# Kernel tuning notes

Hardware: AMD Instinct MI355X
Metric: run time of the kernel (lower is better)

Reference implementation:

```python
import jax, jax.numpy as jnp
import numpy as np


def setup_inputs() -> dict:
    key = jax.random.key(0)
    k1, k2, k3 = jax.random.split(key, 3)
    inputs = jax.random.normal(k1, (1, 39, 39, 64), dtype=jnp.float32)       # successor relevance [1,Hout,Wout,Cout]
    layer_output = jax.random.normal(k2, (1, 160, 160, 4), dtype=jnp.float32)
    layer_weights = jax.random.normal(k3, (8, 8, 4, 64), dtype=jnp.float32)    # conv kernel [f,f,Cin,Cout]
    return {"inputs": inputs, "layer_output": layer_output,
            "layer_weights": layer_weights, "stride": 4, "filter_size": 8}


def _argmax_relevance(inputs, layer_output, layer_weights, stride, filter_size):
    # Faithful, vectorized form of the tf.map_fn over nonzero relevance indices:
    # processing ALL (i,j,c) positions is identical since zero relevance scatters zero.
    x = layer_output[0]
    Hin, Win, Cin = x.shape
    _, Hout, Wout, Cout = inputs.shape
    f, s = filter_size, stride

    # Gather all conv patches: [Hout, Wout, f, f, Cin]
    rows = s * jnp.arange(Hout)[:, None] + jnp.arange(f)[None, :]   # [Hout, f]
    cols = s * jnp.arange(Wout)[:, None] + jnp.arange(f)[None, :]   # [Wout, f]
    patches = x[rows][:, :, cols, :]                                # [Hout, f, Wout, f, Cin]
    patches = jnp.transpose(patches, (0, 2, 1, 3, 4))               # [Hout, Wout, f, f, Cin]

    # Elementwise patch * weight[:, :, :, c] for every output channel, then argmax
    # over the flattened (f, f, Cin) patch — matches Flatten + tf.argmax.
    w = jnp.transpose(layer_weights, (3, 0, 1, 2))                  # [Cout, f, f, Cin]
    prod = patches[:, :, None, :, :, :] * w[None, None]             # [Hout, Wout, Cout, f, f, Cin]
    flat_arg = jnp.argmax(prod.reshape(Hout, Wout, Cout, -1), axis=-1)
    px, py, pc = jnp.unravel_index(flat_arg, (f, f, Cin))           # local patch coords

    gx = px + s * jnp.arange(Hout)[:, None, None]
    gy = py + s * jnp.arange(Wout)[None, :, None]
    flat_idx = (gx * Win + gy) * Cin + pc                           # [Hout, Wout, Cout]

    # Original builds a one-hot mask * relevance per index and reduce_sums -> scatter-add.
    rel = inputs[0]                                                 # relevance read at batch 0
    out = jnp.zeros(Hin * Win * Cin, dtype=inputs.dtype).at[flat_idx.ravel()].add(rel.ravel())
    return out.reshape(1, Hin, Win, Cin)


def reference(inputs, layer_output, layer_weights, stride, filter_size):
    return _argmax_relevance(inputs, layer_output, layer_weights, stride, filter_size)
```

## Files before the change

kernel.cpp:

```cpp
#include <hip/hip_runtime.h>

#define HOUT 39
#define WOUT 39
#define COUT 64
#define HIN  160
#define WIN  160
#define CIN  4
#define F    8
#define S    4

__global__ __launch_bounds__(256) void argmax_rel_kernel(
    const float* __restrict__ rel,
    const float* __restrict__ x,
    const float* __restrict__ w,
    float* __restrict__ out)
{
    const int ij = blockIdx.x;
    const int i  = ij / WOUT;
    const int j  = ij - i * WOUT;
    const int wv = threadIdx.x >> 6;
    const int c  = threadIdx.x & 63;

    const float* xp   = x + ((S * i) * WIN + (S * j)) * CIN;
    const int    kb   = wv * 64;
    const float* row0 = xp + (2 * wv) * (WIN * CIN);
    const float* row1 = row0 + WIN * CIN;
    const float* wp   = w + kb * COUT + c;

    float m0 = -__builtin_inff(), m1 = m0, m2 = m0, m3 = m0;
    int   a0 = 0, a1 = 16, a2 = 32, a3 = 48;

    #pragma unroll
    for (int t = 0; t < 16; ++t) {
        const float p0 = row0[t]      * wp[(t)      * COUT];
        const float p1 = row0[16 + t] * wp[(16 + t) * COUT];
        const float p2 = row1[t]      * wp[(32 + t) * COUT];
        const float p3 = row1[16 + t] * wp[(48 + t) * COUT];
        if (p0 > m0) { m0 = p0; a0 = t; }
        if (p1 > m1) { m1 = p1; a1 = 16 + t; }
        if (p2 > m2) { m2 = p2; a2 = 32 + t; }
        if (p3 > m3) { m3 = p3; a3 = 48 + t; }
    }

    float m = m0; int a = a0;
    if (m1 > m) { m = m1; a = a1; }
    if (m2 > m) { m = m2; a = a2; }
    if (m3 > m) { m = m3; a = a3; }
    a += kb;

    __shared__ float lm[4][COUT];
    __shared__ int   la[4][COUT];
    lm[wv][c] = m;
    la[wv][c] = a;
    __syncthreads();

    if (wv == 0) {
        float bm = lm[0][c]; int ba = la[0][c];
        #pragma unroll
        for (int s = 1; s < 4; ++s) {
            const float sm = lm[s][c];
            if (sm > bm) { bm = sm; ba = la[s][c]; }
        }
        const int px_  = ba >> 5;
        const int rem  = ba & 31;
        const int gx   = S * i + px_;
        const int flat = gx * (WIN * CIN) + (S * j) * CIN + rem;

        atomicAdd(out + flat, rel[ij * COUT + c]);
    }
}

extern "C" void kernel_launch(void* const* d_in, const int* in_sizes, int n_in,
                              void* d_out, int out_size, void* d_ws, size_t ws_size,
                              hipStream_t stream) {
    const float* rel = (const float*)d_in[0];
    const float* x   = (const float*)d_in[1];
    const float* w   = (const float*)d_in[2];
    float* out = (float*)d_out;

    hipMemsetAsync(out, 0, (size_t)out_size * sizeof(float), stream);

    argmax_rel_kernel<<<HOUT * WOUT, 256, 0, stream>>>(rel, x, w, out);
}
```

Before: 18.94 us.

## Remap lanes to channel-quads with float4 weight loads and shuffle argmax reduction

Each lane now handles four output channels and one input-channel slice, loading weights as float4 and a single input value per step. The per-wave argmax is combined across lanes with xor shuffles, using an index tie-break that keeps the first occurrence. This is meant to cut the number of scalar weight loads and to issue wider, coalesced memory accesses. In exchange it adds shuffle reduction work and a conditional write into shared memory.

```diff
diff --git a/kernel.cpp b/kernel.cpp
--- a/kernel.cpp
+++ b/kernel.cpp
@@ -19,54 +19,68 @@
     const int i  = ij / WOUT;
     const int j  = ij - i * WOUT;
     const int wv = threadIdx.x >> 6;
-    const int c  = threadIdx.x & 63;
+    const int l  = threadIdx.x & 63;
+    const int h  = l >> 4;
+    const int cg = (l & 15) << 2;
 
-    const float* xp   = x + ((S * i) * WIN + (S * j)) * CIN;
-    const int    kb   = wv * 64;
-    const float* row0 = xp + (2 * wv) * (WIN * CIN);
-    const float* row1 = row0 + WIN * CIN;
-    const float* wp   = w + kb * COUT + c;
+    const float r = rel[ij * COUT + l];
+
+    const int kb = wv * 64;
+
+    const float4* wp4 = (const float4*)(w + kb * COUT) + l;
+    const float* xb = x + ((S * i + 2 * wv) * WIN + S * j) * CIN + h;
 
     float m0 = -__builtin_inff(), m1 = m0, m2 = m0, m3 = m0;
-    int   a0 = 0, a1 = 16, a2 = 32, a3 = 48;
+    int   a0 = kb + h, a1 = a0, a2 = a0, a3 = a0;
 
     #pragma unroll
     for (int t = 0; t < 16; ++t) {
-        const float p0 = row0[t]      * wp[(t)      * COUT];
-        const float p1 = row0[16 + t] * wp[(16 + t) * COUT];
-        const float p2 = row1[t]      * wp[(32 + t) * COUT];
-        const float p3 = row1[16 + t] * wp[(48 + t) * COUT];
-        if (p0 > m0) { m0 = p0; a0 = t; }
-        if (p1 > m1) { m1 = p1; a1 = 16 + t; }
-        if (p2 > m2) { m2 = p2; a2 = 32 + t; }
-        if (p3 > m3) { m3 = p3; a3 = 48 + t; }
+        const float4 w4 = wp4[t * 64];
+        const float  xv = (t < 8) ? xb[4 * t]
+                                  : xb[WIN * CIN - 32 + 4 * t];
+        const int    k  = kb + 4 * t + h;
+        float p;
+        p = xv * w4.x; if (p > m0) { m0 = p; a0 = k; }
+        p = xv * w4.y; if (p > m1) { m1 = p; a1 = k; }
+        p = xv * w4.z; if (p > m2) { m2 = p; a2 = k; }
+        p = xv * w4.w; if (p > m3) { m3 = p; a3 = k; }
     }
 
-    float m = m0; int a = a0;
-    if (m1 > m) { m = m1; a = a1; }
-    if (m2 > m) { m = m2; a = a2; }
-    if (m3 > m) { m = m3; a = a3; }
-    a += kb;
+    #pragma unroll
+    for (int mask = 16; mask <= 32; mask <<= 1) {
+        const float om0 = __shfl_xor(m0, mask); const int oa0 = __shfl_xor(a0, mask);
+        const float om1 = __shfl_xor(m1, mask); const int oa1 = __shfl_xor(a1, mask);
+        const float om2 = __shfl_xor(m2, mask); const int oa2 = __shfl_xor(a2, mask);
+        const float om3 = __shfl_xor(m3, mask); const int oa3 = __shfl_xor(a3, mask);
+        if (om0 > m0 || (om0 == m0 && oa0 < a0)) { m0 = om0; a0 = oa0; }
+        if (om1 > m1 || (om1 == m1 && oa1 < a1)) { m1 = om1; a1 = oa1; }
+        if (om2 > m2 || (om2 == m2 && oa2 < a2)) { m2 = om2; a2 = oa2; }
+        if (om3 > m3 || (om3 == m3 && oa3 < a3)) { m3 = om3; a3 = oa3; }
+    }
 
     __shared__ float lm[4][COUT];
     __shared__ int   la[4][COUT];
-    lm[wv][c] = m;
-    la[wv][c] = a;
+    if (l < 16) {
+        lm[wv][cg + 0] = m0; la[wv][cg + 0] = a0;
+        lm[wv][cg + 1] = m1; la[wv][cg + 1] = a1;
+        lm[wv][cg + 2] = m2; la[wv][cg + 2] = a2;
+        lm[wv][cg + 3] = m3; la[wv][cg + 3] = a3;
+    }
     __syncthreads();
 
     if (wv == 0) {
-        float bm = lm[0][c]; int ba = la[0][c];
+        float bm = lm[0][l]; int ba = la[0][l];
         #pragma unroll
         for (int s = 1; s < 4; ++s) {
-            const float sm = lm[s][c];
-            if (sm > bm) { bm = sm; ba = la[s][c]; }
+            const float sm = lm[s][l];
+            if (sm > bm) { bm = sm; ba = la[s][l]; }
         }
         const int px_  = ba >> 5;
         const int rem  = ba & 31;
         const int gx   = S * i + px_;
         const int flat = gx * (WIN * CIN) + (S * j) * CIN + rem;
 
-        atomicAdd(out + flat, rel[ij * COUT + c]);
+        atomicAdd(out + flat, r);
     }
 }
 
```

Result: faster. 17.68 us (-6.6%).
